# Kernel tuning notes

Measured on AMD Instinct MI355X. Metric: run time of the kernel, lower is better.

The kernel has to match this reference:

```python
import jax, jax.numpy as jnp
import numpy as np

N = 30000
E = 480000
F_IN = 100
HID = 64
HEADS = 4
NCLS = 47
HC = HEADS * HID  # 256
NEG_SLOPE = 0.2
BN_EPS = 1e-5


def setup_inputs() -> dict:
    key = jax.random.key(0)
    ks = jax.random.split(key, 32)
    s = 0.1
    inp = {
        'x': jax.random.normal(ks[0], (N, F_IN), jnp.float32),
        'edge_index': jax.random.randint(ks[1], (2, E), 0, N, jnp.int32),
        # layer 0: GATConv(F_IN -> HID, heads, concat=True)
        'w0': jax.random.normal(ks[2], (F_IN, HC), jnp.float32) * s,
        'as0': jax.random.normal(ks[3], (HEADS, HID), jnp.float32) * s,
        'ad0': jax.random.normal(ks[4], (HEADS, HID), jnp.float32) * s,
        'b0': jnp.zeros((HC,), jnp.float32),
        'sw0': jax.random.normal(ks[5], (F_IN, HC), jnp.float32) * s,
        'sb0': jnp.zeros((HC,), jnp.float32),
        'g0': jnp.ones((HC,), jnp.float32),
        'be0': jnp.zeros((HC,), jnp.float32),
        # layer 1: GATConv(HC -> HID, heads, concat=True)
        'w1': jax.random.normal(ks[6], (HC, HC), jnp.float32) * s,
        'as1': jax.random.normal(ks[7], (HEADS, HID), jnp.float32) * s,
        'ad1': jax.random.normal(ks[8], (HEADS, HID), jnp.float32) * s,
        'b1': jnp.zeros((HC,), jnp.float32),
        'sw1': jax.random.normal(ks[9], (HC, HC), jnp.float32) * s,
        'sb1': jnp.zeros((HC,), jnp.float32),
        'g1': jnp.ones((HC,), jnp.float32),
        'be1': jnp.zeros((HC,), jnp.float32),
        # layer 2: GATConv(HC -> NCLS, heads, concat=False)
        'w2': jax.random.normal(ks[10], (HC, HEADS * NCLS), jnp.float32) * s,
        'as2': jax.random.normal(ks[11], (HEADS, NCLS), jnp.float32) * s,
        'ad2': jax.random.normal(ks[12], (HEADS, NCLS), jnp.float32) * s,
        'b2': jnp.zeros((NCLS,), jnp.float32),
        'sw2': jax.random.normal(ks[13], (HC, NCLS), jnp.float32) * s,
        'sb2': jnp.zeros((NCLS,), jnp.float32),
    }
    return inp


def gat_conv(x, src, dst, W, a_src, a_dst, bias, heads, out_ch, concat):
    # shared linear for src/dst (PyG GATConv with int in_channels)
    h = (x @ W).reshape(N, heads, out_ch)           # [N,H,C]
    al_s = jnp.sum(h * a_src, axis=-1)              # [N,H]
    al_d = jnp.sum(h * a_dst, axis=-1)              # [N,H]
    e = jax.nn.leaky_relu(al_s[src] + al_d[dst], NEG_SLOPE)  # [E,H]
    # segment (per-destination) softmax
    m = jax.ops.segment_max(e, dst, num_segments=N)
    e = jnp.exp(e - m[dst])
    den = jax.ops.segment_sum(e, dst, num_segments=N)
    alpha = e / (den[dst] + 1e-16)                  # [E,H]
    msg = h[src] * alpha[:, :, None]                # [E,H,C]
    out = jax.ops.segment_sum(msg, dst, num_segments=N)  # [N,H,C]
    out = out.reshape(N, heads * out_ch) if concat else out.mean(axis=1)
    return out + bias


def batch_norm(x, gamma, beta):
    mu = jnp.mean(x, axis=0)
    var = jnp.var(x, axis=0)
    return gamma * (x - mu) * jax.lax.rsqrt(var + BN_EPS) + beta


def reference(x, edge_index, w0, as0, ad0, b0, sw0, sb0, g0, be0,
              w1, as1, ad1, b1, sw1, sb1, g1, be1,
              w2, as2, ad2, b2, sw2, sb2):
    src, dst = edge_index[0], edge_index[1]
    # layer 0
    h = gat_conv(x, src, dst, w0, as0, ad0, b0, HEADS, HID, True)
    h = h + x @ sw0 + sb0
    h = jax.nn.elu(batch_norm(h, g0, be0))
    # layer 1
    h2 = gat_conv(h, src, dst, w1, as1, ad1, b1, HEADS, HID, True)
    h2 = h2 + h @ sw1 + sb1
    h2 = jax.nn.elu(batch_norm(h2, g1, be1))
    # layer 2 (concat=False -> mean over heads)
    out = gat_conv(h2, src, dst, w2, as2, ad2, b2, HEADS, NCLS, False)
    out = out + h2 @ sw2 + sb2
    return jax.nn.log_softmax(out, axis=-1)
```

## Files before the change

kernel.cpp:

```cpp
#include <hip/hip_runtime.h>
#include <math.h>

#define NN 30000
#define EE 480000
#define FIN 100
#define NCLS 47
#define SCAN_B 118

typedef unsigned short ushortt;
typedef __attribute__((ext_vector_type(8))) short bf16x8;
typedef __attribute__((ext_vector_type(4))) float f32x4;
typedef __attribute__((ext_vector_type(2))) float f32x2;

__device__ unsigned char g_H8[(size_t)NN * 256];
__device__ ushortt g_Sb[(size_t)NN * 256];
__device__ float   g_S2[(size_t)NN * 48];
__device__ ushortt g_Fb[(size_t)NN * 256];
__device__ ushortt g_Xb[(size_t)NN * 128];
__device__ ushortt g_Wc0[512 * 128];
__device__ ushortt g_Wc1[512 * 256];
__device__ ushortt g_Wc2[235 * 256];
__device__ float g_als[NN * 4];
__device__ float g_ald[NN * 4];
__device__ int   g_rowptr[NN + 1];
__device__ int   g_counts[NN];
__device__ int   g_bsum[128];
__device__ int   g_esrc[EE];
__device__ float g_stat[1024];

__device__ __forceinline__ float wsum(float v) {
#pragma unroll
  for (int o = 32; o > 0; o >>= 1) v += __shfl_xor(v, o, 64);
  return v;
}
__device__ __forceinline__ float lrelu(float x) { return x > 0.f ? x : 0.2f * x; }
__device__ __forceinline__ ushortt f2bf(float f) {
  unsigned int u = __float_as_uint(f);
  unsigned int r = u + 0x7FFF + ((u >> 16) & 1);
  return (ushortt)(r >> 16);
}
__device__ __forceinline__ float bf2f(ushortt u) {
  return __uint_as_float(((unsigned int)u) << 16);
}
__device__ __forceinline__ unsigned int pk4_fp8(float f0, float f1, float f2, float f3) {
  unsigned int r = 0;
  r = __builtin_amdgcn_cvt_pk_fp8_f32(f0, f1, r, false);
  r = __builtin_amdgcn_cvt_pk_fp8_f32(f2, f3, r, true);
  return r;
}
__device__ __forceinline__ int swz(int row, int k) {
  return (k & ~63) | ((((k >> 3) & 7) ^ (row & 7)) << 3) | (k & 7);
}
__device__ __forceinline__ void glds16(const ushortt* gp, ushortt* lp) {
  __builtin_amdgcn_global_load_lds(
      (const __attribute__((address_space(1))) unsigned int*)gp,
      (__attribute__((address_space(3))) unsigned int*)lp, 16, 0, 0);
}

__global__ void count_kernel(const int* __restrict__ dst) {
  int e = blockIdx.x * blockDim.x + threadIdx.x;
  if (e < EE) atomicAdd(&g_counts[dst[e]], 1);
}
__global__ void scan1_kernel() {
  int i = blockIdx.x * 256 + threadIdx.x;
  int v = (i < NN) ? g_counts[i] : 0;
  __shared__ int sh[4];
  float fv = (float)v;
  fv = wsum(fv);
  if ((threadIdx.x & 63) == 0) sh[threadIdx.x >> 6] = (int)fv;
  __syncthreads();
  if (threadIdx.x == 0) g_bsum[blockIdx.x] = sh[0] + sh[1] + sh[2] + sh[3];
}
__global__ void scan2_kernel() {
  __shared__ int sh[128];
  int t = threadIdx.x;
  int v = (t < SCAN_B) ? g_bsum[t] : 0;
  sh[t] = v;
  __syncthreads();
  for (int off = 1; off < 128; off <<= 1) {
    int x = (t >= off) ? sh[t - off] : 0;
    __syncthreads();
    sh[t] += x;
    __syncthreads();
  }
  g_bsum[t] = sh[t] - v;
}
__global__ void scan3_kernel() {
  __shared__ int sh[256];
  int t = threadIdx.x;
  int i = blockIdx.x * 256 + t;
  int v = (i < NN) ? g_counts[i] : 0;
  sh[t] = v;
  __syncthreads();
  for (int off = 1; off < 256; off <<= 1) {
    int x = (t >= off) ? sh[t - off] : 0;
    __syncthreads();
    sh[t] += x;
    __syncthreads();
  }
  if (i < NN) {
    g_rowptr[i] = g_bsum[blockIdx.x] + sh[t] - v;
    g_counts[i] = 0;
  }
  if (i == NN - 1) g_rowptr[NN] = EE;
}
__global__ void scatter_kernel(const int* __restrict__ dst, const int* __restrict__ src) {
  int e = blockIdx.x * blockDim.x + threadIdx.x;
  if (e < EE) {
    int d = dst[e];
    int pos = g_rowptr[d] + atomicAdd(&g_counts[d], 1);
    g_esrc[pos] = src[e];
  }
}

#define CW0 (512 * 128)
#define CW1 (512 * 256)
#define CW2 (235 * 256)
__global__ void conv_kernel(const float* __restrict__ w0, const float* __restrict__ sw0,
                            const float* __restrict__ w1, const float* __restrict__ sw1,
                            const float* __restrict__ w2, const float* __restrict__ sw2,
                            const float* __restrict__ x) {
  int i = blockIdx.x * blockDim.x + threadIdx.x;
  if (i < CW0) {
    int m = i >> 7, k = i & 127;
    float v = 0.f;
    if (k < FIN) v = (m < 256) ? w0[k * 256 + m] : sw0[k * 256 + (m - 256)];
    g_Wc0[(m << 7) | swz(m, k)] = f2bf(v);
    return;
  }
  i -= CW0;
  if (i < CW1) {
    int m = i >> 8, k = i & 255;
    float v = (m < 256) ? w1[k * 256 + m] : sw1[k * 256 + (m - 256)];
    g_Wc1[(m << 8) | swz(m, k)] = f2bf(v);
    return;
  }
  i -= CW1;
  if (i < CW2) {
    int m = i >> 8, k = i & 255;
    float v = (m < 188) ? w2[(size_t)k * 188 + m] : sw2[(size_t)k * 47 + (m - 188)];
    g_Wc2[(m << 8) | swz(m, k)] = f2bf(v);
    return;
  }
  i -= CW2;
  if (i < NN * 128) {
    int r = i >> 7, k = i & 127;
    g_Xb[(r << 7) | swz(r, k)] = (k < FIN) ? f2bf(x[r * FIN + k]) : 0;
    return;
  }
  i -= NN * 128;
  if (i < NN) {
    g_counts[i] = 0;
    return;
  }
  i -= NN;
  if (i < 1024) g_stat[i] = 0.f;
}

__global__ __launch_bounds__(256) void mfma_gemm(
    const ushortt* __restrict__ A, const ushortt* __restrict__ Wt,
    unsigned char* __restrict__ out8, ushortt* __restrict__ out2b,
    float* __restrict__ out2f,
    int nrows, int Kp, int M, int S, int ld8, int ld2,
    const float* __restrict__ bias2, int pad47,
    const float* __restrict__ a_s, const float* __restrict__ a_d,
    float* __restrict__ alsp, float* __restrict__ aldp) {
  __shared__ __align__(16) ushortt smem[12288];
  ushortt* As = smem;
  ushortt* Ws = smem + 64 * 64;
  float* Ls = (float*)smem;
  int t = threadIdx.x;
  int wave = t >> 6, lane = t & 63;
  int row0 = blockIdx.y * 64, col0 = blockIdx.x * 128;
  int wr = wave >> 1, wc = wave & 1;
  int m16 = lane & 15, q = lane >> 4;
  int rin8 = lane >> 3;
  int koff = (lane & 7) * 8;

  f32x4 acc[2][4];
#pragma unroll
  for (int i = 0; i < 2; i++)
#pragma unroll
    for (int j = 0; j < 4; j++) acc[i][j] = (f32x4){0.f, 0.f, 0.f, 0.f};

  for (int k0 = 0; k0 < Kp; k0 += 64) {
#pragma unroll
    for (int r = 0; r < 2; r++) {
      int lrow = wave * 16 + r * 8;
      int ga = min(row0 + lrow + rin8, nrows - 1);
      glds16(A + (size_t)ga * Kp + k0 + koff, &As[lrow * 64]);
    }
#pragma unroll
    for (int r = 0; r < 4; r++) {
      int lrow = wave * 32 + r * 8;
      int gw = min(col0 + lrow + rin8, M - 1);
      glds16(Wt + (size_t)gw * Kp + k0 + koff, &Ws[lrow * 64]);
    }
    __syncthreads();
#pragma unroll
    for (int c = 0; c < 2; c++) {
      bf16x8 af[2], bf[4];
#pragma unroll
      for (int i = 0; i < 2; i++) {
        int row = wr * 32 + i * 16 + m16;
        int ch = (c * 4 + q) ^ (row & 7);
        af[i] = *(const bf16x8*)(&As[row * 64 + ch * 8]);
      }
#pragma unroll
      for (int i = 0; i < 4; i++) {
        int row = wc * 64 + i * 16 + m16;
        int ch = (c * 4 + q) ^ (row & 7);
        bf[i] = *(const bf16x8*)(&Ws[row * 64 + ch * 8]);
      }
#pragma unroll
      for (int rt = 0; rt < 2; rt++)
#pragma unroll
        for (int ct = 0; ct < 4; ct++)
          acc[rt][ct] = __builtin_amdgcn_mfma_f32_16x16x32_bf16(af[rt], bf[ct], acc[rt][ct], 0, 0, 0);
    }
    __syncthreads();
  }

  bool all1 = (!pad47) && (col0 + 128 <= S);
  bool all2 = (col0 >= S);
  int row8 = t >> 3, seg = t & 7;
#pragma unroll
  for (int p = 0; p < 2; p++) {
    __syncthreads();
    if (wr == p) {
#pragma unroll
      for (int rt = 0; rt < 2; rt++) {
#pragma unroll
        for (int ctt = 0; ctt < 4; ctt++) {
#pragma unroll
          for (int reg = 0; reg < 4; reg++) {
            int rloc = rt * 16 + q * 4 + reg;
            Ls[rloc * 132 + wc * 64 + ctt * 16 + m16] = acc[rt][ctt][reg];
          }
        }
      }
    }
    __syncthreads();
    int grow = row0 + p * 32 + row8;
    if (grow < nrows) {
      const float* lrow = Ls + row8 * 132 + seg * 16;
      int cbase = col0 + seg * 16;
      if (all1) {
        unsigned int q8[4];
#pragma unroll
        for (int kk = 0; kk < 4; kk++)
          q8[kk] = pk4_fp8(lrow[kk * 4], lrow[kk * 4 + 1], lrow[kk * 4 + 2], lrow[kk * 4 + 3]);
        uint4 v8 = {q8[0], q8[1], q8[2], q8[3]};
        *(uint4*)(out8 + (size_t)grow * ld8 + cbase) = v8;
        float s_p = 0.f, d_p = 0.f;
#pragma unroll
        for (int kk = 0; kk < 16; kk++) {
          s_p += lrow[kk] * a_s[cbase + kk];
          d_p += lrow[kk] * a_d[cbase + kk];
        }
        s_p += __shfl_xor(s_p, 1, 64); s_p += __shfl_xor(s_p, 2, 64);
        d_p += __shfl_xor(d_p, 1, 64); d_p += __shfl_xor(d_p, 2, 64);
        if ((seg & 3) == 0) {
          int head = cbase >> 6;
          alsp[grow * 4 + head] = s_p;
          aldp[grow * 4 + head] = d_p;
        }
      } else if (all2) {
        const float* brow = bias2 + (cbase - S);
        ushortt* orow = out2b + (size_t)grow * ld2 + (cbase - S);
        unsigned int pk[8];
#pragma unroll
        for (int kk = 0; kk < 8; kk++) {
          unsigned int lo = f2bf(lrow[kk * 2] + brow[kk * 2]);
          unsigned int hi = f2bf(lrow[kk * 2 + 1] + brow[kk * 2 + 1]);
          pk[kk] = lo | (hi << 16);
        }
        uint4 v0 = {pk[0], pk[1], pk[2], pk[3]};
        uint4 v1 = {pk[4], pk[5], pk[6], pk[7]};
        *(uint4*)(orow) = v0;
        *(uint4*)(orow + 8) = v1;
      } else {
        float pa0 = 0.f, pa1 = 0.f, pd0 = 0.f, pd1 = 0.f;
        int h0 = cbase / 47;
        for (int kk = 0; kk < 16; kk++) {
          int c = cbase + kk;
          if (c >= M) break;
          float v = lrow[kk];
          if (c < S) {
            int hd = c / 47, ch = c - hd * 47;
            int c1 = hd * 48 + ch;
            out8[(size_t)grow * ld8 + c1] =
                (unsigned char)(pk4_fp8(v, 0.f, 0.f, 0.f) & 0xFF);
            if (ch == 46) out8[(size_t)grow * ld8 + c1 + 1] = 0;
            float sw = a_s[hd * 47 + ch], dw = a_d[hd * 47 + ch];
            if (hd == h0) { pa0 += v * sw; pd0 += v * dw; }
            else { pa1 += v * sw; pd1 += v * dw; }
          } else {
            out2f[(size_t)grow * ld2 + (c - S)] = v + bias2[c - S];
          }
        }
        if (pad47 && cbase < S) {
          if (pa0 != 0.f || pd0 != 0.f) {
            atomicAdd(&alsp[grow * 4 + h0], pa0);
            atomicAdd(&aldp[grow * 4 + h0], pd0);
          }
          if ((pa1 != 0.f || pd1 != 0.f) && h0 + 1 < 4) {
            atomicAdd(&alsp[grow * 4 + h0 + 1], pa1);
            atomicAdd(&aldp[grow * 4 + h0 + 1], pd1);
          }
        }
      }
    }
  }
}

__global__ __launch_bounds__(256) void attn_kernel(const unsigned char* __restrict__ H8,
                                                   const float* __restrict__ bias,
                                                   ushortt* __restrict__ Sb) {
  __shared__ __align__(16) float p_sh[4 * 256];
  __shared__ int s_sh[4 * 64];
  int w = threadIdx.x >> 6, lane = threadIdx.x & 63;
  int n = blockIdx.x * 4 + w;
  float* pw = p_sh + w * 256;
  int* sw_ = s_sh + w * 64;
  int rs = g_rowptr[n], deg = g_rowptr[n + 1] - rs;
  float4 ald = *(const float4*)(g_ald + n * 4);
  int q = lane >> 4;
  float den0 = 0, den1 = 0, den2 = 0, den3 = 0;
  float a0 = 0, a1 = 0, a2 = 0, a3 = 0;
  for (int base = 0; base < deg; base += 64) {
    int j = base + lane;
    float p0 = 0, p1 = 0, p2 = 0, p3 = 0;
    int s = 0;
    if (j < deg) {
      s = g_esrc[rs + j];
      float4 av = *(const float4*)(g_als + s * 4);
      p0 = __expf(lrelu(av.x + ald.x)); den0 += p0;
      p1 = __expf(lrelu(av.y + ald.y)); den1 += p1;
      p2 = __expf(lrelu(av.z + ald.z)); den2 += p2;
      p3 = __expf(lrelu(av.w + ald.w)); den3 += p3;
    }
    pw[lane * 4 + 0] = p0; pw[lane * 4 + 1] = p1;
    pw[lane * 4 + 2] = p2; pw[lane * 4 + 3] = p3;
    sw_[lane] = s;
    int cnt = min(64, deg - base);
    for (int jj = 0; jj < cnt; jj++) {
      int ss = sw_[jj];
      float p = pw[jj * 4 + q];
      unsigned int hv = *(const unsigned int*)(H8 + (size_t)ss * 256 + 4 * lane);
      f32x2 lo = __builtin_amdgcn_cvt_pk_f32_fp8(hv, false);
      f32x2 hi = __builtin_amdgcn_cvt_pk_f32_fp8(hv, true);
      a0 += p * lo.x;
      a1 += p * lo.y;
      a2 += p * hi.x;
      a3 += p * hi.y;
    }
  }
  den0 = wsum(den0); den1 = wsum(den1); den2 = wsum(den2); den3 = wsum(den3);
  float denq = (q == 0) ? den0 : (q == 1) ? den1 : (q == 2) ? den2 : den3;
  float inv = 1.f / (denq + 1e-16f);
  size_t o = (size_t)n * 256 + 4 * lane;
  ushort4 sv = *(const ushort4*)(Sb + o);
  float4 bv = *(const float4*)(bias + 4 * lane);
  ushort4 ov;
  ov.x = f2bf(a0 * inv + bv.x + bf2f(sv.x));
  ov.y = f2bf(a1 * inv + bv.y + bf2f(sv.y));
  ov.z = f2bf(a2 * inv + bv.z + bf2f(sv.z));
  ov.w = f2bf(a3 * inv + bv.w + bf2f(sv.w));
  *(ushort4*)(Sb + o) = ov;
}

__global__ __launch_bounds__(256) void attn2_kernel(const unsigned char* __restrict__ H8,
                                                    const float* __restrict__ bias,
                                                    const float* __restrict__ S2,
                                                    float* __restrict__ out) {
  __shared__ __align__(16) float p_sh[4 * 256];
  __shared__ int s_sh[4 * 64];
  __shared__ float xh[4][4][48];
  int w = threadIdx.x >> 6, lane = threadIdx.x & 63;
  int n = blockIdx.x * 4 + w;
  float* pw = p_sh + w * 256;
  int* sw_ = s_sh + w * 64;
  int rs = g_rowptr[n], deg = g_rowptr[n + 1] - rs;
  float4 ald = *(const float4*)(g_ald + n * 4);
  int head = lane / 12;
  float den0 = 0, den1 = 0, den2 = 0, den3 = 0;
  float a0 = 0, a1 = 0, a2 = 0, a3 = 0;
  for (int base = 0; base < deg; base += 64) {
    int j = base + lane;
    float p0 = 0, p1 = 0, p2 = 0, p3 = 0;
    int s = 0;
    if (j < deg) {
      s = g_esrc[rs + j];
      float4 av = *(const float4*)(g_als + s * 4);
      p0 = __expf(lrelu(av.x + ald.x)); den0 += p0;
      p1 = __expf(lrelu(av.y + ald.y)); den1 += p1;
      p2 = __expf(lrelu(av.z + ald.z)); den2 += p2;
      p3 = __expf(lrelu(av.w + ald.w)); den3 += p3;
    }
    pw[lane * 4 + 0] = p0; pw[lane * 4 + 1] = p1;
    pw[lane * 4 + 2] = p2; pw[lane * 4 + 3] = p3;
    sw_[lane] = s;
    int cnt = min(64, deg - base);
    if (lane < 48) {
      for (int jj = 0; jj < cnt; jj++) {
        int ss = sw_[jj];
        float p = pw[jj * 4 + head];
        unsigned int hv = *(const unsigned int*)(H8 + (size_t)ss * 192 + lane * 4);
        f32x2 lo = __builtin_amdgcn_cvt_pk_f32_fp8(hv, false);
        f32x2 hi = __builtin_amdgcn_cvt_pk_f32_fp8(hv, true);
        a0 += p * lo.x;
        a1 += p * lo.y;
        a2 += p * hi.x;
        a3 += p * hi.y;
      }
    }
  }
  den0 = wsum(den0); den1 = wsum(den1); den2 = wsum(den2); den3 = wsum(den3);
  if (lane < 48) {
    float dh = (head == 0) ? den0 : (head == 1) ? den1 : (head == 2) ? den2 : den3;
    float inv = 1.f / (dh + 1e-16f);
    int chin = (lane % 12) * 4;
    xh[w][head][chin + 0] = a0 * inv;
    xh[w][head][chin + 1] = a1 * inv;
    xh[w][head][chin + 2] = a2 * inv;
    xh[w][head][chin + 3] = a3 * inv;
  }
  float v = 0.f;
  if (lane < NCLS)
    v = 0.25f * (xh[w][0][lane] + xh[w][1][lane] + xh[w][2][lane] + xh[w][3][lane]) +
        bias[lane] + S2[(size_t)n * NCLS + lane];
  float mv = (lane < NCLS) ? v : -INFINITY;
#pragma unroll
  for (int o = 32; o > 0; o >>= 1) mv = fmaxf(mv, __shfl_xor(mv, o, 64));
  float ex = (lane < NCLS) ? __expf(v - mv) : 0.f;
  float s = wsum(ex);
  if (lane < NCLS) out[(size_t)n * NCLS + lane] = v - mv - logf(s);
}

__global__ void bn_stats_kernel(const ushortt* __restrict__ Sb, float* __restrict__ stat) {
  int c = threadIdx.x;
  int rows = (NN + gridDim.x - 1) / gridDim.x;
  int r0 = blockIdx.x * rows, r1 = min(r0 + rows, NN);
  float s = 0, q = 0;
  for (int r = r0; r < r1; r++) {
    float v = bf2f(Sb[(size_t)r * 256 + c]);
    s += v;
    q += v * v;
  }
  atomicAdd(&stat[c], s);
  atomicAdd(&stat[256 + c], q);
}
__global__ void bn_norm_kernel(const ushortt* __restrict__ Sb, const float* __restrict__ gamma,
                               const float* __restrict__ beta, const float* __restrict__ stat,
                               float* __restrict__ zs, float* __restrict__ zd) {
  int i = blockIdx.x * blockDim.x + threadIdx.x;
  if (i >= NN * 256) return;
  int c = i & 255;
  int r = i >> 8;
  float mu = stat[c] * (1.f / NN);
  float var = stat[256 + c] * (1.f / NN) - mu * mu;
  float v = (bf2f(Sb[i]) - mu) * rsqrtf(var + 1e-5f) * gamma[c] + beta[c];
  v = v > 0.f ? v : (__expf(v) - 1.f);
  g_Fb[(r << 8) | swz(r, c)] = f2bf(v);
  if (zs && i < NN * 4) {
    zs[i] = 0.f;
    zd[i] = 0.f;
  }
}

extern "C" void kernel_launch(void* const* d_in, const int* in_sizes, int n_in,
                              void* d_out, int out_size, void* d_ws, size_t ws_size,
                              hipStream_t stream) {
  const float* x = (const float*)d_in[0];
  const int* ei = (const int*)d_in[1];
  const int* src = ei;
  const int* dst = ei + EE;
  const float* w0 = (const float*)d_in[2];
  const float* as0 = (const float*)d_in[3];
  const float* ad0 = (const float*)d_in[4];
  const float* b0 = (const float*)d_in[5];
  const float* sw0 = (const float*)d_in[6];
  const float* sb0 = (const float*)d_in[7];
  const float* gm0 = (const float*)d_in[8];
  const float* be0 = (const float*)d_in[9];
  const float* w1 = (const float*)d_in[10];
  const float* as1 = (const float*)d_in[11];
  const float* ad1 = (const float*)d_in[12];
  const float* b1 = (const float*)d_in[13];
  const float* sw1 = (const float*)d_in[14];
  const float* sb1 = (const float*)d_in[15];
  const float* gm1 = (const float*)d_in[16];
  const float* be1 = (const float*)d_in[17];
  const float* w2 = (const float*)d_in[18];
  const float* as2 = (const float*)d_in[19];
  const float* ad2 = (const float*)d_in[20];
  const float* b2 = (const float*)d_in[21];
  const float* sw2 = (const float*)d_in[22];
  const float* sb2 = (const float*)d_in[23];
  float* out = (float*)d_out;

  ushortt *Sb, *Fb, *Xb, *Wc0, *Wc1, *Wc2;
  unsigned char* H8;
  float *S2, *als, *ald, *stat;
  hipGetSymbolAddress((void**)&H8, HIP_SYMBOL(g_H8));
  hipGetSymbolAddress((void**)&Sb, HIP_SYMBOL(g_Sb));
  hipGetSymbolAddress((void**)&S2, HIP_SYMBOL(g_S2));
  hipGetSymbolAddress((void**)&Fb, HIP_SYMBOL(g_Fb));
  hipGetSymbolAddress((void**)&Xb, HIP_SYMBOL(g_Xb));
  hipGetSymbolAddress((void**)&Wc0, HIP_SYMBOL(g_Wc0));
  hipGetSymbolAddress((void**)&Wc1, HIP_SYMBOL(g_Wc1));
  hipGetSymbolAddress((void**)&Wc2, HIP_SYMBOL(g_Wc2));
  hipGetSymbolAddress((void**)&als, HIP_SYMBOL(g_als));
  hipGetSymbolAddress((void**)&ald, HIP_SYMBOL(g_ald));
  hipGetSymbolAddress((void**)&stat, HIP_SYMBOL(g_stat));

  conv_kernel<<<(CW0 + CW1 + CW2 + NN * 128 + NN + 1024 + 255) / 256, 256, 0, stream>>>(
      w0, sw0, w1, sw1, w2, sw2, x);

  count_kernel<<<(EE + 255) / 256, 256, 0, stream>>>(dst);
  scan1_kernel<<<SCAN_B, 256, 0, stream>>>();
  scan2_kernel<<<1, 128, 0, stream>>>();
  scan3_kernel<<<SCAN_B, 256, 0, stream>>>();
  scatter_kernel<<<(EE + 255) / 256, 256, 0, stream>>>(dst, src);

  const int gy = (NN + 63) / 64;
  const int ga = NN / 4;

  mfma_gemm<<<dim3(4, gy), 256, 0, stream>>>(Xb, Wc0, H8, Sb, nullptr, NN, 128, 512, 256,
                                             256, 256, sb0, 0, as0, ad0, als, ald);
  attn_kernel<<<ga, 256, 0, stream>>>(H8, b0, Sb);
  bn_stats_kernel<<<240, 256, 0, stream>>>(Sb, stat);
  bn_norm_kernel<<<(NN * 256 + 255) / 256, 256, 0, stream>>>(Sb, gm0, be0, stat,
                                                             nullptr, nullptr);

  mfma_gemm<<<dim3(4, gy), 256, 0, stream>>>(Fb, Wc1, H8, Sb, nullptr, NN, 256, 512, 256,
                                             256, 256, sb1, 0, as1, ad1, als, ald);
  attn_kernel<<<ga, 256, 0, stream>>>(H8, b1, Sb);
  bn_stats_kernel<<<240, 256, 0, stream>>>(Sb, stat + 512);
  bn_norm_kernel<<<(NN * 256 + 255) / 256, 256, 0, stream>>>(Sb, gm1, be1, stat + 512,
                                                             als, ald);

  mfma_gemm<<<dim3(2, gy), 256, 0, stream>>>(Fb, Wc2, H8, nullptr, S2, NN, 256, 235, 188,
                                             192, 47, sb2, 1, as2, ad2, als, ald);
  attn2_kernel<<<ga, 256, 0, stream>>>(H8, b2, S2, out);
}
```

Before: 437.1 us.

## Fuse BN statistics into attention, merge CSR build kernels, vectorize BN normalize

```diff
diff --git a/kernel.cpp b/kernel.cpp
--- a/kernel.cpp
+++ b/kernel.cpp
@@ -5,10 +5,11 @@
 #define EE 480000
 #define FIN 100
 #define NCLS 47
-#define SCAN_B 118
+#define NCOPY 16
 
 typedef unsigned short ushortt;
 typedef __attribute__((ext_vector_type(8))) short bf16x8;
+typedef __attribute__((ext_vector_type(8))) unsigned short us8;
 typedef __attribute__((ext_vector_type(4))) float f32x4;
 typedef __attribute__((ext_vector_type(2))) float f32x2;
 
@@ -24,9 +25,9 @@
 __device__ float g_ald[NN * 4];
 __device__ int   g_rowptr[NN + 1];
 __device__ int   g_counts[NN];
-__device__ int   g_bsum[128];
+__device__ int   g_cur[NN];
 __device__ int   g_esrc[EE];
-__device__ float g_stat[1024];
+__device__ float g_stat[2 * NCOPY * 512];
 
 __device__ __forceinline__ float wsum(float v) {
 #pragma unroll
@@ -57,69 +58,14 @@
       (__attribute__((address_space(3))) unsigned int*)lp, 16, 0, 0);
 }
 
-__global__ void count_kernel(const int* __restrict__ dst) {
-  int e = blockIdx.x * blockDim.x + threadIdx.x;
-  if (e < EE) atomicAdd(&g_counts[dst[e]], 1);
-}
-__global__ void scan1_kernel() {
-  int i = blockIdx.x * 256 + threadIdx.x;
-  int v = (i < NN) ? g_counts[i] : 0;
-  __shared__ int sh[4];
-  float fv = (float)v;
-  fv = wsum(fv);
-  if ((threadIdx.x & 63) == 0) sh[threadIdx.x >> 6] = (int)fv;
-  __syncthreads();
-  if (threadIdx.x == 0) g_bsum[blockIdx.x] = sh[0] + sh[1] + sh[2] + sh[3];
-}
-__global__ void scan2_kernel() {
-  __shared__ int sh[128];
-  int t = threadIdx.x;
-  int v = (t < SCAN_B) ? g_bsum[t] : 0;
-  sh[t] = v;
-  __syncthreads();
-  for (int off = 1; off < 128; off <<= 1) {
-    int x = (t >= off) ? sh[t - off] : 0;
-    __syncthreads();
-    sh[t] += x;
-    __syncthreads();
-  }
-  g_bsum[t] = sh[t] - v;
-}
-__global__ void scan3_kernel() {
-  __shared__ int sh[256];
-  int t = threadIdx.x;
-  int i = blockIdx.x * 256 + t;
-  int v = (i < NN) ? g_counts[i] : 0;
-  sh[t] = v;
-  __syncthreads();
-  for (int off = 1; off < 256; off <<= 1) {
-    int x = (t >= off) ? sh[t - off] : 0;
-    __syncthreads();
-    sh[t] += x;
-    __syncthreads();
-  }
-  if (i < NN) {
-    g_rowptr[i] = g_bsum[blockIdx.x] + sh[t] - v;
-    g_counts[i] = 0;
-  }
-  if (i == NN - 1) g_rowptr[NN] = EE;
-}
-__global__ void scatter_kernel(const int* __restrict__ dst, const int* __restrict__ src) {
-  int e = blockIdx.x * blockDim.x + threadIdx.x;
-  if (e < EE) {
-    int d = dst[e];
-    int pos = g_rowptr[d] + atomicAdd(&g_counts[d], 1);
-    g_esrc[pos] = src[e];
-  }
-}
-
 #define CW0 (512 * 128)
 #define CW1 (512 * 256)
 #define CW2 (235 * 256)
+#define STATZ (2 * NCOPY * 512)
 __global__ void conv_kernel(const float* __restrict__ w0, const float* __restrict__ sw0,
                             const float* __restrict__ w1, const float* __restrict__ sw1,
                             const float* __restrict__ w2, const float* __restrict__ sw2,
-                            const float* __restrict__ x) {
+                            const float* __restrict__ x, const int* __restrict__ dst) {
   int i = blockIdx.x * blockDim.x + threadIdx.x;
   if (i < CW0) {
     int m = i >> 7, k = i & 127;
@@ -149,12 +95,55 @@
     return;
   }
   i -= NN * 128;
-  if (i < NN) {
-    g_counts[i] = 0;
+  if (i < STATZ) {
+    g_stat[i] = 0.f;
     return;
   }
-  i -= NN;
-  if (i < 1024) g_stat[i] = 0.f;
+  i -= STATZ;
+  if (i < EE) atomicAdd(&g_counts[dst[i]], 1);
+}
+
+__global__ __launch_bounds__(1024) void scan_kernel() {
+  __shared__ int sh[1024];
+  int t = threadIdx.x;
+  int base = t * 30;
+  int cnt[30];
+  int sum = 0;
+#pragma unroll
+  for (int k = 0; k < 30; k++) {
+    int i = base + k;
+    int v = (i < NN) ? g_counts[i] : 0;
+    cnt[k] = v;
+    sum += v;
+  }
+  sh[t] = sum;
+  __syncthreads();
+  for (int off = 1; off < 1024; off <<= 1) {
+    int xv = (t >= off) ? sh[t - off] : 0;
+    __syncthreads();
+    sh[t] += xv;
+    __syncthreads();
+  }
+  int run = sh[t] - sum;
+#pragma unroll
+  for (int k = 0; k < 30; k++) {
+    int i = base + k;
+    if (i < NN) {
+      g_rowptr[i] = run;
+      run += cnt[k];
+      g_counts[i] = 0;
+      g_cur[i] = 0;
+    }
+  }
+  if (t == 0) g_rowptr[NN] = EE;
+}
+__global__ void scatter_kernel(const int* __restrict__ dst, const int* __restrict__ src) {
+  int e = blockIdx.x * blockDim.x + threadIdx.x;
+  if (e < EE) {
+    int d = dst[e];
+    int pos = g_rowptr[d] + atomicAdd(&g_cur[d], 1);
+    g_esrc[pos] = src[e];
+  }
 }
 
 __global__ __launch_bounds__(256) void mfma_gemm(
@@ -316,9 +305,12 @@
 
 __global__ __launch_bounds__(256) void attn_kernel(const unsigned char* __restrict__ H8,
                                                    const float* __restrict__ bias,
-                                                   ushortt* __restrict__ Sb) {
+                                                   ushortt* __restrict__ Sb,
+                                                   float* __restrict__ statp) {
   __shared__ __align__(16) float p_sh[4 * 256];
   __shared__ int s_sh[4 * 64];
+  __shared__ float rs_[4 * 256];
+  __shared__ float rq_[4 * 256];
   int w = threadIdx.x >> 6, lane = threadIdx.x & 63;
   int n = blockIdx.x * 4 + w;
   float* pw = p_sh + w * 256;
@@ -368,6 +360,17 @@
   ov.z = f2bf(a2 * inv + bv.z + bf2f(sv.z));
   ov.w = f2bf(a3 * inv + bv.w + bf2f(sv.w));
   *(ushort4*)(Sb + o) = ov;
+  float v0 = bf2f(ov.x), v1 = bf2f(ov.y), v2 = bf2f(ov.z), v3 = bf2f(ov.w);
+  int cb = w * 256 + 4 * lane;
+  rs_[cb + 0] = v0; rs_[cb + 1] = v1; rs_[cb + 2] = v2; rs_[cb + 3] = v3;
+  rq_[cb + 0] = v0 * v0; rq_[cb + 1] = v1 * v1; rq_[cb + 2] = v2 * v2; rq_[cb + 3] = v3 * v3;
+  __syncthreads();
+  int c = threadIdx.x;
+  float s = rs_[c] + rs_[256 + c] + rs_[512 + c] + rs_[768 + c];
+  float qq = rq_[c] + rq_[256 + c] + rq_[512 + c] + rq_[768 + c];
+  int copy = blockIdx.x & (NCOPY - 1);
+  atomicAdd(&statp[copy * 512 + c], s);
+  atomicAdd(&statp[copy * 512 + 256 + c], qq);
 }
 
 __global__ __launch_bounds__(256) void attn2_kernel(const unsigned char* __restrict__ H8,
@@ -438,34 +441,53 @@
   if (lane < NCLS) out[(size_t)n * NCLS + lane] = v - mv - logf(s);
 }
 
-__global__ void bn_stats_kernel(const ushortt* __restrict__ Sb, float* __restrict__ stat) {
-  int c = threadIdx.x;
+__global__ __launch_bounds__(256) void bn_norm_kernel(const ushortt* __restrict__ Sb,
+                                                      const float* __restrict__ gamma,
+                                                      const float* __restrict__ beta,
+                                                      const float* __restrict__ statp,
+                                                      float* __restrict__ zs,
+                                                      float* __restrict__ zd) {
+  __shared__ float sc_sh[256], off_sh[256];
+  int t = threadIdx.x;
+  float s = 0.f, qq = 0.f;
+#pragma unroll
+  for (int k = 0; k < NCOPY; k++) {
+    s += statp[k * 512 + t];
+    qq += statp[k * 512 + 256 + t];
+  }
+  float mu = s * (1.f / NN);
+  float var = qq * (1.f / NN) - mu * mu;
+  float rg = rsqrtf(var + 1e-5f) * gamma[t];
+  sc_sh[t] = rg;
+  off_sh[t] = beta[t] - mu * rg;
+  __syncthreads();
+  if (zs) {
+    for (int i = blockIdx.x * 256 + t; i < NN * 4; i += gridDim.x * 256) {
+      zs[i] = 0.f;
+      zd[i] = 0.f;
+    }
+  }
   int rows = (NN + gridDim.x - 1) / gridDim.x;
   int r0 = blockIdx.x * rows, r1 = min(r0 + rows, NN);
-  float s = 0, q = 0;
-  for (int r = r0; r < r1; r++) {
-    float v = bf2f(Sb[(size_t)r * 256 + c]);
-    s += v;
-    q += v * v;
-  }
-  atomicAdd(&stat[c], s);
-  atomicAdd(&stat[256 + c], q);
-}
-__global__ void bn_norm_kernel(const ushortt* __restrict__ Sb, const float* __restrict__ gamma,
-                               const float* __restrict__ beta, const float* __restrict__ stat,
-                               float* __restrict__ zs, float* __restrict__ zd) {
-  int i = blockIdx.x * blockDim.x + threadIdx.x;
-  if (i >= NN * 256) return;
-  int c = i & 255;
-  int r = i >> 8;
-  float mu = stat[c] * (1.f / NN);
-  float var = stat[256 + c] * (1.f / NN) - mu * mu;
-  float v = (bf2f(Sb[i]) - mu) * rsqrtf(var + 1e-5f) * gamma[c] + beta[c];
-  v = v > 0.f ? v : (__expf(v) - 1.f);
-  g_Fb[(r << 8) | swz(r, c)] = f2bf(v);
-  if (zs && i < NN * 4) {
-    zs[i] = 0.f;
-    zd[i] = 0.f;
+  int chunk = t & 31;
+  int ro = t >> 5;
+  float scv[8], ofv[8];
+#pragma unroll
+  for (int k = 0; k < 8; k++) {
+    scv[k] = sc_sh[chunk * 8 + k];
+    ofv[k] = off_sh[chunk * 8 + k];
+  }
+  for (int r = r0 + ro; r < r1; r += 8) {
+    us8 xv = *(const us8*)(Sb + (size_t)r * 256 + chunk * 8);
+    us8 yv;
+#pragma unroll
+    for (int k = 0; k < 8; k++) {
+      float v = bf2f((ushortt)xv[k]) * scv[k] + ofv[k];
+      v = v > 0.f ? v : (__expf(v) - 1.f);
+      yv[k] = f2bf(v);
+    }
+    int c8 = (chunk & 24) | ((chunk & 7) ^ (r & 7));
+    *(us8*)(g_Fb + ((size_t)r << 8) + c8 * 8) = yv;
   }
 }
 
@@ -515,13 +537,10 @@
   hipGetSymbolAddress((void**)&ald, HIP_SYMBOL(g_ald));
   hipGetSymbolAddress((void**)&stat, HIP_SYMBOL(g_stat));
 
-  conv_kernel<<<(CW0 + CW1 + CW2 + NN * 128 + NN + 1024 + 255) / 256, 256, 0, stream>>>(
-      w0, sw0, w1, sw1, w2, sw2, x);
-
-  count_kernel<<<(EE + 255) / 256, 256, 0, stream>>>(dst);
-  scan1_kernel<<<SCAN_B, 256, 0, stream>>>();
-  scan2_kernel<<<1, 128, 0, stream>>>();
-  scan3_kernel<<<SCAN_B, 256, 0, stream>>>();
+  const int convN = CW0 + CW1 + CW2 + NN * 128 + STATZ + EE;
+  conv_kernel<<<(convN + 255) / 256, 256, 0, stream>>>(w0, sw0, w1, sw1, w2, sw2, x, dst);
+
+  scan_kernel<<<1, 1024, 0, stream>>>();
   scatter_kernel<<<(EE + 255) / 256, 256, 0, stream>>>(dst, src);
 
   const int gy = (NN + 63) / 64;
@@ -529,17 +548,13 @@
 
   mfma_gemm<<<dim3(4, gy), 256, 0, stream>>>(Xb, Wc0, H8, Sb, nullptr, NN, 128, 512, 256,
                                              256, 256, sb0, 0, as0, ad0, als, ald);
-  attn_kernel<<<ga, 256, 0, stream>>>(H8, b0, Sb);
-  bn_stats_kernel<<<240, 256, 0, stream>>>(Sb, stat);
-  bn_norm_kernel<<<(NN * 256 + 255) / 256, 256, 0, stream>>>(Sb, gm0, be0, stat,
-                                                             nullptr, nullptr);
+  attn_kernel<<<ga, 256, 0, stream>>>(H8, b0, Sb, stat);
+  bn_norm_kernel<<<480, 256, 0, stream>>>(Sb, gm0, be0, stat, nullptr, nullptr);
 
   mfma_gemm<<<dim3(4, gy), 256, 0, stream>>>(Fb, Wc1, H8, Sb, nullptr, NN, 256, 512, 256,
                                              256, 256, sb1, 0, as1, ad1, als, ald);
-  attn_kernel<<<ga, 256, 0, stream>>>(H8, b1, Sb);
-  bn_stats_kernel<<<240, 256, 0, stream>>>(Sb, stat + 512);
-  bn_norm_kernel<<<(NN * 256 + 255) / 256, 256, 0, stream>>>(Sb, gm1, be1, stat + 512,
-                                                             als, ald);
+  attn_kernel<<<ga, 256, 0, stream>>>(H8, b1, Sb, stat + NCOPY * 512);
+  bn_norm_kernel<<<480, 256, 0, stream>>>(Sb, gm1, be1, stat + NCOPY * 512, als, ald);
 
   mfma_gemm<<<dim3(2, gy), 256, 0, stream>>>(Fb, Wc2, H8, nullptr, S2, NN, 256, 235, 188,
                                              192, 47, sb2, 1, as2, ad2, als, ald);
```

Result: no change. 429.6 us (-1.7%).
